# Kernel optimization log

Measured on AMD Instinct MI355X. Metric: run time of the kernel, lower is better.

The kernel has to match this reference:

```python
import jax, jax.numpy as jnp
import numpy as np

N_ANCH = 100800   # 3 * (160^2 + 80^2 + 40^2), YOLOv5 @ 1280
NUM_CLS = 80
IMG_HW = 1280
MAX_DETS = 300    # fixed padding for jit-compatible NMS output
OUT = 224
SCORE_THRESH = 0.1
IOU_THRESH = 0.45
ALLOWED = jnp.array([1, 2, 3, 4, 6, 8, 17, 18, 44], dtype=jnp.int32)
MEAN = jnp.array([0.485, 0.456, 0.406], dtype=jnp.float32).reshape(1, 3, 1, 1)
STD = jnp.array([0.229, 0.224, 0.225], dtype=jnp.float32).reshape(1, 3, 1, 1)


def setup_inputs() -> dict:
    key = jax.random.key(0)
    k1, k2, k3, k4, k5 = jax.random.split(key, 5)
    # realistic YOLO-style raw predictions: cx,cy in-image, modest w,h, gaussian class logits
    cxcy = jax.random.uniform(k1, (1, 2, N_ANCH), dtype=jnp.float32) * IMG_HW
    wh = jax.random.uniform(k2, (1, 2, N_ANCH), dtype=jnp.float32) * 256.0 + 8.0
    obj = jax.random.uniform(k3, (1, 1, N_ANCH), dtype=jnp.float32)
    logits = jax.random.normal(k4, (1, NUM_CLS, N_ANCH), dtype=jnp.float32)
    raw_pred = jnp.concatenate([cxcy, wh, obj, logits], axis=1)  # [1, 5+C, N]
    image = jax.random.uniform(k5, (1, 3, IMG_HW, IMG_HW), dtype=jnp.float32)
    return {"raw_pred": raw_pred, "image": image}


def _pairwise_iou(b):
    # b: [K,4] xyxy
    area = (b[:, 2] - b[:, 0]) * (b[:, 3] - b[:, 1])
    lt = jnp.maximum(b[:, None, :2], b[None, :, :2])
    rb = jnp.minimum(b[:, None, 2:], b[None, :, 2:])
    wh = jnp.clip(rb - lt, 0.0)
    inter = wh[..., 0] * wh[..., 1]
    union = area[:, None] + area[None, :] - inter
    return inter / jnp.maximum(union, 1e-9)


def _nms_keep(iou, valid):
    # greedy NMS over score-sorted boxes; returns boolean keep mask [K]
    K = iou.shape[0]
    idx = jnp.arange(K)

    def body(i, keep):
        suppress = keep[i] & (iou[i] > IOU_THRESH) & (idx > i)
        return keep & ~suppress

    return jax.lax.fori_loop(0, K, body, valid)


def _roi_align(image_chw, boxes):
    # torchvision roi_align, aligned=True, one sample per bin at the bin center
    # (sampling_ratio fixed to 1; see notes). image_chw: [3,H,W], boxes: [M,4]
    C, H, W = image_chw.shape
    grid = (jnp.arange(OUT, dtype=jnp.float32) + 0.5) / OUT  # fractional bin centers

    def one(box):
        x1, y1, x2, y2 = box
        xs = x1 - 0.5 + grid * (x2 - x1)  # [OUT], aligned=True half-pixel offset
        ys = y1 - 0.5 + grid * (y2 - y1)
        vx = (xs >= -1.0) & (xs <= W)
        vy = (ys >= -1.0) & (ys <= H)
        xc = jnp.clip(xs, 0.0, W - 1)
        yc = jnp.clip(ys, 0.0, H - 1)
        x0 = jnp.floor(xc).astype(jnp.int32)
        y0 = jnp.floor(yc).astype(jnp.int32)
        x1i = jnp.minimum(x0 + 1, W - 1)
        y1i = jnp.minimum(y0 + 1, H - 1)
        lx = xc - x0
        ly = yc - y0
        # bilinear gather: [3, OUT, OUT]
        v00 = image_chw[:, y0[:, None], x0[None, :]]
        v01 = image_chw[:, y0[:, None], x1i[None, :]]
        v10 = image_chw[:, y1i[:, None], x0[None, :]]
        v11 = image_chw[:, y1i[:, None], x1i[None, :]]
        top = v00 * (1.0 - lx) + v01 * lx
        bot = v10 * (1.0 - lx) + v11 * lx
        val = top * (1.0 - ly)[None, :, None] + bot * ly[None, :, None]
        return jnp.where(vy[None, :, None] & vx[None, None, :], val, 0.0)

    return jax.vmap(one)(boxes)


def _forward(raw_pred, image):
    x = raw_pred[0].T  # [N, 5+C]
    cx, cy, w, h = x[:, 0], x[:, 1], x[:, 2], x[:, 3]
    boxes = jnp.stack([cx - w / 2, cy - h / 2, cx + w / 2, cy + h / 2], axis=1)
    cls_logits = x[:, 5:]
    scores = cls_logits.max(axis=1)
    classes = cls_logits.argmax(axis=1).astype(jnp.int32) + 1
    # score + allowed-class filter (mask form)
    mask = (scores > SCORE_THRESH) & jnp.isin(classes, ALLOWED)
    masked_scores = jnp.where(mask, scores, jnp.finfo(scores.dtype).min)
    top_scores, top_idx = jax.lax.top_k(masked_scores, MAX_DETS)  # sorted desc
    top_boxes = boxes[top_idx]
    top_classes = classes[top_idx]
    valid = mask[top_idx]
    # greedy NMS over padded top-K candidates
    keep = _nms_keep(_pairwise_iou(top_boxes), valid)
    final_boxes = jnp.where(keep[:, None], top_boxes, 0.0)
    final_scores = jnp.where(keep, top_scores, 0.0)
    final_classes = jnp.where(keep, top_classes, 0)
    # crops: full image first, then RoIAlign crops, normalized once
    full_crop = jax.image.resize(image, (1, 3, OUT, OUT), method='linear', antialias=False)
    roi_crops = _roi_align(image[0], final_boxes)  # [K,3,224,224]
    roi_crops = jnp.where(keep[:, None, None, None], roi_crops, 0.0)
    all_crops = jnp.concatenate([full_crop, roi_crops], axis=0)  # [K+1,3,224,224]
    all_crops = (all_crops - MEAN) / STD
    return final_boxes, final_scores, final_classes, all_crops, keep


def reference(raw_pred, image):
    return _forward(raw_pred, image)
```

## Files before the change

kernel.cpp:

```cpp
#include <hip/hip_runtime.h>
#include <stdint.h>

#define N_ANCH   100800
#define NUM_CLS  80
#define IMG_HW   1280
#define MAX_DETS 300
#define OUTSZ    224
#define CAND_CAP 4096
#define LIST_CAP 16384

#define OFF_BOXES   0
#define OFF_SCORES  1200
#define OFF_CLASSES 1500
#define OFF_CROPS   1800
#define CROPS_ELEMS (301 * 3 * 224 * 224)
#define OFF_KEEP    (OFF_CROPS + CROPS_ELEMS)

#define SC_CNT    0
#define SC_CAND   64

typedef float f32x4 __attribute__((ext_vector_type(4)));

__device__ __forceinline__ uint32_t fkey(float f) {
    uint32_t u = __float_as_uint(f);
    return (u & 0x80000000u) ? ~u : (u | 0x80000000u);
}
__device__ __forceinline__ float unfkey(uint32_t k) {
    uint32_t u = (k & 0x80000000u) ? (k & 0x7fffffffu) : ~k;
    return __uint_as_float(u);
}

__global__ void k_score(const float* __restrict__ rp,
                        unsigned long long* __restrict__ cand,
                        uint32_t* __restrict__ cnt) {
    int gid = blockIdx.x * 256 + threadIdx.x;
    int grp = gid >> 3;
    int cp  = gid & 7;
    bool in = (grp < N_ANCH / 4);
    int a4 = in ? grp * 4 : 0;

    float best[4] = {-3.402823466e38f, -3.402823466e38f, -3.402823466e38f, -3.402823466e38f};
    int   bc[4]   = {0, 0, 0, 0};
    #pragma unroll
    for (int k = 0; k < 10; ++k) {
        int c = cp + 8 * k;
        float4 v = *(const float4*)&rp[(size_t)(5 + c) * N_ANCH + a4];
        if (v.x > best[0]) { best[0] = v.x; bc[0] = c; }
        if (v.y > best[1]) { best[1] = v.y; bc[1] = c; }
        if (v.z > best[2]) { best[2] = v.z; bc[2] = c; }
        if (v.w > best[3]) { best[3] = v.w; bc[3] = c; }
    }
    #pragma unroll
    for (int m = 1; m < 8; m <<= 1) {
        #pragma unroll
        for (int j = 0; j < 4; ++j) {
            float ob = __shfl_xor(best[j], m);
            int   oc = __shfl_xor(bc[j], m);
            if (ob > best[j] || (ob == best[j] && oc < bc[j])) { best[j] = ob; bc[j] = oc; }
        }
    }

    const unsigned long long AM =
        (1ULL << 1) | (1ULL << 2) | (1ULL << 3) | (1ULL << 4) | (1ULL << 6) |
        (1ULL << 8) | (1ULL << 17) | (1ULL << 18) | (1ULL << 44);
    unsigned long long pk[4];
    int cnt_loc = 0;
    bool lead = (cp == 0) && in;
    #pragma unroll
    for (int k = 0; k < 4; ++k) {
        int cls = bc[k] + 1;
        bool mk = lead && (best[k] > 0.1f) && (cls < 64) && ((AM >> cls) & 1ULL);
        uint32_t low = ((0x1FFFFu ^ (uint32_t)(a4 + k)) << 7) | (uint32_t)cls;
        pk[k] = mk ? (((unsigned long long)fkey(best[k]) << 32) | low) : 0ull;
        cnt_loc += mk ? 1 : 0;
    }

    int inc = cnt_loc;
    #pragma unroll
    for (int d = 1; d < 64; d <<= 1) {
        int vv = __shfl_up(inc, d);
        if ((threadIdx.x & 63) >= d) inc += vv;
    }
    int total = __shfl(inc, 63);
    uint32_t base = 0u;
    if (((threadIdx.x & 63) == 63) && total > 0) base = atomicAdd(cnt, (uint32_t)total);
    base = (uint32_t)__shfl((int)base, 63);
    uint32_t pos = base + (uint32_t)(inc - cnt_loc);
    #pragma unroll
    for (int k = 0; k < 4; ++k) {
        if (pk[k]) {
            if (pos < LIST_CAP) cand[pos] = pk[k];
            ++pos;
        }
    }
}

__global__ void __launch_bounds__(1024) k_detect(const float* __restrict__ rp,
                                                 const unsigned long long* __restrict__ cand,
                                                 const uint32_t* __restrict__ cnt_p,
                                                 float* __restrict__ out) {
    __shared__ uint32_t lhist[16384];
    __shared__ uint32_t ssum[1024];
    __shared__ uint32_t swave[16];
    __shared__ int      sh_thr;
    __shared__ uint32_t s_cnt;
    __shared__ unsigned long long sb[CAND_CAP];
    __shared__ unsigned long long top[MAX_DETS];
    __shared__ float sbx[MAX_DETS][4];
    __shared__ float sscore[MAX_DETS];
    __shared__ int   scls[MAX_DETS];
    __shared__ __align__(8) uint32_t sup[MAX_DETS][10];
    __shared__ __align__(8) uint32_t kw[10];
    __shared__ __align__(8) uint32_t rnz[10];
    int t = threadIdx.x;
    int nl = min((int)(*cnt_p), LIST_CAP);

    #pragma unroll
    for (int i = 0; i < 16; ++i) lhist[t + i * 1024] = 0u;
    if (t == 0) s_cnt = 0u;
    __syncthreads();
    for (int i = t; i < nl; i += 1024)
        atomicAdd(&lhist[(uint32_t)(cand[i] >> 50)], 1u);
    __syncthreads();

    const uint4* h4 = (const uint4*)(&lhist[t * 16]);
    uint4 v0 = h4[0], v1 = h4[1], v2 = h4[2], v3 = h4[3];
    uint32_t s = v0.x + v0.y + v0.z + v0.w + v1.x + v1.y + v1.z + v1.w +
                 v2.x + v2.y + v2.z + v2.w + v3.x + v3.y + v3.z + v3.w;
    ssum[t] = s;
    uint32_t ws = s;
    #pragma unroll
    for (int m = 32; m; m >>= 1) ws += __shfl_xor(ws, m);
    if ((t & 63) == 0) swave[t >> 6] = ws;
    __syncthreads();
    if (t == 0) {
        uint32_t acc = 0; int wsel = -1;
        for (int w = 15; w >= 0; --w) {
            uint32_t v = swave[w];
            if (acc + v >= (uint32_t)MAX_DETS) { wsel = w; break; }
            acc += v;
        }
        int thr = 0;
        if (wsel >= 0) {
            int tsel = -1;
            for (int tg = wsel * 64 + 63; tg >= wsel * 64; --tg) {
                uint32_t v = ssum[tg];
                if (acc + v >= (uint32_t)MAX_DETS) { tsel = tg; break; }
                acc += v;
            }
            for (int b = tsel * 16 + 15; b >= tsel * 16; --b) {
                acc += lhist[b];
                if (acc >= (uint32_t)MAX_DETS) { thr = b; break; }
            }
        }
        sh_thr = thr;
    }
    __syncthreads();

    uint32_t thr = (uint32_t)sh_thr;
    for (int i = t; i < nl; i += 1024) {
        unsigned long long key = cand[i];
        if ((uint32_t)(key >> 50) >= thr) {
            uint32_t pos = atomicAdd(&s_cnt, 1u);
            if (pos < CAND_CAP) sb[pos] = key;
        }
    }
    __syncthreads();
    int n = min((int)s_cnt, CAND_CAP);

    if (t < MAX_DETS) top[t] = 0ull;
    for (int i = t; i < MAX_DETS * 10; i += 1024) ((uint32_t*)sup)[i] = 0u;
    if (t < 10) { kw[t] = 0u; rnz[t] = 0u; }
    __syncthreads();

    for (int i = t; i < n; i += 1024) {
        unsigned long long key = sb[i];
        int rank = 0;
        for (int j = 0; j < n; ++j) rank += (sb[j] > key) ? 1 : 0;
        if (rank < MAX_DETS) top[rank] = key;
    }
    __syncthreads();

    if (t < MAX_DETS) {
        unsigned long long key = top[t];
        bool valid = (key != 0ull);
        float score = 0.f; int cls = 0;
        float b0 = 0.f, b1 = 0.f, b2 = 0.f, b3 = 0.f;
        if (valid) {
            uint32_t low = (uint32_t)key;
            uint32_t a = 0x1FFFFu ^ ((low >> 7) & 0x1FFFFu);
            cls = (int)(low & 0x7Fu);
            score = unfkey((uint32_t)(key >> 32));
            float cx = rp[a], cy = rp[N_ANCH + a];
            float w = rp[2 * N_ANCH + a], h = rp[3 * N_ANCH + a];
            b0 = cx - w * 0.5f; b1 = cy - h * 0.5f;
            b2 = cx + w * 0.5f; b3 = cy + h * 0.5f;
            atomicOr(&kw[t >> 5], 1u << (t & 31));
        }
        sbx[t][0] = b0; sbx[t][1] = b1; sbx[t][2] = b2; sbx[t][3] = b3;
        sscore[t] = score; scls[t] = cls;
    }
    __syncthreads();

    for (int p = t; p < MAX_DETS * MAX_DETS; p += 1024) {
        int i = p / MAX_DETS, j = p % MAX_DETS;
        if (j > i) {
            float ax1 = sbx[i][0], ay1 = sbx[i][1], ax2 = sbx[i][2], ay2 = sbx[i][3];
            float bx1 = sbx[j][0], by1 = sbx[j][1], bx2 = sbx[j][2], by2 = sbx[j][3];
            float areaA = (ax2 - ax1) * (ay2 - ay1);
            float areaB = (bx2 - bx1) * (by2 - by1);
            float ltx = fmaxf(ax1, bx1), lty = fmaxf(ay1, by1);
            float rbx = fminf(ax2, bx2), rby = fminf(ay2, by2);
            float iw = fmaxf(rbx - ltx, 0.f), ih = fmaxf(rby - lty, 0.f);
            float inter = iw * ih;
            float uni = areaA + areaB - inter;
            float iou = inter / fmaxf(uni, 1e-9f);
            if (iou > 0.45f) {
                atomicOr(&sup[i][j >> 5], 1u << (j & 31));
                atomicOr(&rnz[i >> 5], 1u << (i & 31));
            }
        }
    }
    __syncthreads();

    if (t == 0) {
        unsigned long long kwr[5], rnzr[5];
        const unsigned long long* kq = (const unsigned long long*)kw;
        const unsigned long long* rq = (const unsigned long long*)rnz;
        #pragma unroll
        for (int w = 0; w < 5; ++w) { kwr[w] = kq[w]; rnzr[w] = rq[w]; }
        #pragma unroll
        for (int sblk = 0; sblk < 5; ++sblk) {
            int lim = (sblk == 4) ? (MAX_DETS - 4 * 64) : 64;
            for (int i2 = 0; i2 < lim; ++i2) {
                if (((kwr[sblk] >> i2) & 1ull) && ((rnzr[sblk] >> i2) & 1ull)) {
                    int i = sblk * 64 + i2;
                    const unsigned long long* row = (const unsigned long long*)&sup[i][0];
                    kwr[0] &= ~row[0]; kwr[1] &= ~row[1]; kwr[2] &= ~row[2];
                    kwr[3] &= ~row[3]; kwr[4] &= ~row[4];
                }
            }
        }
        unsigned long long* kqo = (unsigned long long*)kw;
        #pragma unroll
        for (int w = 0; w < 5; ++w) kqo[w] = kwr[w];
    }
    __syncthreads();

    if (t < MAX_DETS) {
        bool kp = (kw[t >> 5] >> (t & 31)) & 1u;
        out[OFF_BOXES + t * 4 + 0] = kp ? sbx[t][0] : 0.f;
        out[OFF_BOXES + t * 4 + 1] = kp ? sbx[t][1] : 0.f;
        out[OFF_BOXES + t * 4 + 2] = kp ? sbx[t][2] : 0.f;
        out[OFF_BOXES + t * 4 + 3] = kp ? sbx[t][3] : 0.f;
        out[OFF_SCORES + t]  = kp ? sscore[t] : 0.f;
        out[OFF_CLASSES + t] = kp ? (float)scls[t] : 0.f;
        out[OFF_KEEP + t]    = kp ? 1.f : 0.f;
    }
}

#define RPB    16
#define TROWS  22
#define TPITCH 272

__device__ __forceinline__ float bilerp_g(const float* __restrict__ ch, float xc, float yc) {
    int x0 = (int)floorf(xc), y0 = (int)floorf(yc);
    int x1 = min(x0 + 1, IMG_HW - 1), y1 = min(y0 + 1, IMG_HW - 1);
    float lx = xc - (float)x0, ly = yc - (float)y0;
    float v00 = ch[y0 * IMG_HW + x0], v01 = ch[y0 * IMG_HW + x1];
    float v10 = ch[y1 * IMG_HW + x0], v11 = ch[y1 * IMG_HW + x1];
    return (v00 * (1.f - lx) + v01 * lx) * (1.f - ly) +
           (v10 * (1.f - lx) + v11 * lx) * ly;
}

__global__ void k_crops(const float* __restrict__ img, float* __restrict__ out) {
    __shared__ float tile[TROWS * TPITCH];
    int bx = blockIdx.x;
    int nc = blockIdx.y;
    int n = nc / 3, c = nc - n * 3;
    int t = threadIdx.x;
    int rl = t / 14;
    int xs14 = t - rl * 14;
    bool act = (t < 224);
    int oy = bx * RPB + rl;
    int ox0 = xs14 * 16;
    const float meanv[3] = {0.485f, 0.456f, 0.406f};
    const float stdv[3]  = {0.229f, 0.224f, 0.225f};
    float mean = meanv[c], rstd = 1.0f / stdv[c];
    const float* ch = img + (size_t)c * (IMG_HW * IMG_HW);
    f32x4 v[4];

    if (n == 0) {
        if (act) {
            float sy = ((float)oy + 0.5f) * (1280.0f / 224.0f) - 0.5f;
            #pragma unroll
            for (int k = 0; k < 16; ++k) {
                float sx = ((float)(ox0 + k) + 0.5f) * (1280.0f / 224.0f) - 0.5f;
                v[k >> 2][k & 3] = (bilerp_g(ch, sx, sy) - mean) * rstd;
            }
        }
    } else {
        float kp = out[OFF_KEEP + (n - 1)];
        if (kp == 0.f) {
            float z = (0.f - mean) * rstd;
            #pragma unroll
            for (int k4 = 0; k4 < 4; ++k4) v[k4] = (f32x4){z, z, z, z};
        } else {
            float4 bxv = *(const float4*)&out[OFF_BOXES + (n - 1) * 4];
            float x1b = bxv.x, y1b = bxv.y, x2b = bxv.z, y2b = bxv.w;
            float bw = x2b - x1b, bh = y2b - y1b;
            float ys0 = y1b - 0.5f + (((float)(bx * RPB) + 0.5f) / 224.0f) * bh;
            float ys1 = y1b - 0.5f + (((float)(bx * RPB + RPB - 1) + 0.5f) / 224.0f) * bh;
            int iy_min = (int)floorf(fminf(fmaxf(ys0, 0.f), 1279.f));
            int iy_max = min((int)floorf(fminf(fmaxf(ys1, 0.f), 1279.f)) + 1, IMG_HW - 1);
            float xs0 = x1b - 0.5f + (0.5f / 224.0f) * bw;
            float xs1 = x1b - 0.5f + (223.5f / 224.0f) * bw;
            int ix_min = (int)floorf(fminf(fmaxf(xs0, 0.f), 1279.f));
            int ix_max = min((int)floorf(fminf(fmaxf(xs1, 0.f), 1279.f)) + 1, IMG_HW - 1);
            int ix_al = ix_min & ~3;
            int rows = iy_max - iy_min + 1;
            int w4   = (ix_max - ix_al + 4) >> 2;
            int total = rows * w4;
            float winv = 1.0f / (float)w4;
            for (int i = t; i < total; i += 256) {
                int r  = (int)((float)i * winv);
                int cc = i - r * w4;
                if (cc < 0)        { r--; cc += w4; }
                else if (cc >= w4) { r++; cc -= w4; }
                int gy = iy_min + r;
                int px = ix_al + cc * 4;
                const float* src = ch + (size_t)gy * IMG_HW + px;
                float4 val;
                if ((px + 3 < IMG_HW) || (gy < IMG_HW - 1) || (c < 2)) {
                    val = *(const float4*)src;
                } else {
                    val.x = src[0];
                    val.y = src[min(1, IMG_HW - 1 - px)];
                    val.z = src[min(2, IMG_HW - 1 - px)];
                    val.w = src[min(3, IMG_HW - 1 - px)];
                }
                *(float4*)&tile[r * TPITCH + cc * 4] = val;
            }
            __syncthreads();
            if (act) {
                float gy = ((float)oy + 0.5f) / 224.0f;
                float ys = y1b - 0.5f + gy * bh;
                bool vy = (ys >= -1.0f) && (ys <= 1280.0f);
                float ycl = fminf(fmaxf(ys, 0.f), 1279.f);
                int y0 = (int)floorf(ycl);
                int y1i = min(y0 + 1, IMG_HW - 1);
                float ly = ycl - (float)y0;
                int ry0 = (y0 - iy_min) * TPITCH - ix_al;
                int ry1 = (y1i - iy_min) * TPITCH - ix_al;
                #pragma unroll
                for (int k = 0; k < 16; ++k) {
                    float gx = ((float)(ox0 + k) + 0.5f) / 224.0f;
                    float xs = x1b - 0.5f + gx * bw;
                    bool vx = (xs >= -1.0f) && (xs <= 1280.0f);
                    float xcl = fminf(fmaxf(xs, 0.f), 1279.f);
                    int x0 = (int)floorf(xcl);
                    int x1i = min(x0 + 1, IMG_HW - 1);
                    float lx = xcl - (float)x0;
                    float v00 = tile[ry0 + x0], v01 = tile[ry0 + x1i];
                    float v10 = tile[ry1 + x0], v11 = tile[ry1 + x1i];
                    float val = (v00 * (1.f - lx) + v01 * lx) * (1.f - ly) +
                                (v10 * (1.f - lx) + v11 * lx) * ly;
                    if (!(vx && vy)) val = 0.f;
                    v[k >> 2][k & 3] = (val - mean) * rstd;
                }
            }
        }
    }
    if (act) {
        float* dst = out + OFF_CROPS + (size_t)nc * (OUTSZ * OUTSZ) + (size_t)oy * OUTSZ + ox0;
        #pragma unroll
        for (int k4 = 0; k4 < 4; ++k4)
            __builtin_nontemporal_store(v[k4], (f32x4*)(dst + k4 * 4));
    }
}

extern "C" void kernel_launch(void* const* d_in, const int* in_sizes, int n_in,
                              void* d_out, int out_size, void* d_ws, size_t ws_size,
                              hipStream_t stream) {
    (void)in_sizes; (void)n_in; (void)out_size; (void)d_ws; (void)ws_size;
    const float* rp  = (const float*)d_in[0];
    const float* img = (const float*)d_in[1];
    float* out = (float*)d_out;
    char* sbase = (char*)d_out + (size_t)OFF_CROPS * sizeof(float);
    uint32_t* cnt = (uint32_t*)(sbase + SC_CNT);
    unsigned long long* cand = (unsigned long long*)(sbase + SC_CAND);

    hipMemsetAsync(sbase, 0, 64, stream);
    k_score<<<(N_ANCH / 4 * 8 + 255) / 256, 256, 0, stream>>>(rp, cand, cnt);
    k_detect<<<1, 1024, 0, stream>>>(rp, cand, cnt, out);
    dim3 grid(14, 903);
    k_crops<<<grid, 256, 0, stream>>>(img, out);
}
```

Before: 391.6 us.

## Remap crop kernel to four outputs per thread and add interior fast path

Crop blocks now cover 256 threads times four contiguous outputs, replacing sixteen outputs per thread over sixteen rows. The grid grows from 14 to 49 blocks per channel-crop, and the staged shared tile shrinks to about six source rows. This raises parallelism and cuts per-thread register use. A branch-free interior path using FMA-based bilinear interpolation skips clamping and validity checks when the box lies fully inside the image. The cost is more blocks and more redundant tile staging per output row.

Result: faster. 344.0 us (-12.2%).

```diff
diff --git a/kernel.cpp b/kernel.cpp
--- a/kernel.cpp
+++ b/kernel.cpp
@@ -259,8 +259,7 @@
     }
 }
 
-#define RPB    16
-#define TROWS  22
+#define TROWS  8
 #define TPITCH 272
 
 __device__ __forceinline__ float bilerp_g(const float* __restrict__ ch, float xc, float yc) {
@@ -279,42 +278,40 @@
     int nc = blockIdx.y;
     int n = nc / 3, c = nc - n * 3;
     int t = threadIdx.x;
-    int rl = t / 14;
-    int xs14 = t - rl * 14;
-    bool act = (t < 224);
-    int oy = bx * RPB + rl;
-    int ox0 = xs14 * 16;
+    int q = bx * 256 + t;
+    int oy = q / 56;
+    int ox0 = (q - oy * 56) * 4;
     const float meanv[3] = {0.485f, 0.456f, 0.406f};
     const float stdv[3]  = {0.229f, 0.224f, 0.225f};
     float mean = meanv[c], rstd = 1.0f / stdv[c];
     const float* ch = img + (size_t)c * (IMG_HW * IMG_HW);
-    f32x4 v[4];
+    f32x4 v;
 
     if (n == 0) {
-        if (act) {
-            float sy = ((float)oy + 0.5f) * (1280.0f / 224.0f) - 0.5f;
-            #pragma unroll
-            for (int k = 0; k < 16; ++k) {
-                float sx = ((float)(ox0 + k) + 0.5f) * (1280.0f / 224.0f) - 0.5f;
-                v[k >> 2][k & 3] = (bilerp_g(ch, sx, sy) - mean) * rstd;
-            }
+        float sy = ((float)oy + 0.5f) * (1280.0f / 224.0f) - 0.5f;
+        #pragma unroll
+        for (int k = 0; k < 4; ++k) {
+            float sx = ((float)(ox0 + k) + 0.5f) * (1280.0f / 224.0f) - 0.5f;
+            v[k] = (bilerp_g(ch, sx, sy) - mean) * rstd;
         }
     } else {
         float kp = out[OFF_KEEP + (n - 1)];
         if (kp == 0.f) {
             float z = (0.f - mean) * rstd;
-            #pragma unroll
-            for (int k4 = 0; k4 < 4; ++k4) v[k4] = (f32x4){z, z, z, z};
+            v = (f32x4){z, z, z, z};
         } else {
             float4 bxv = *(const float4*)&out[OFF_BOXES + (n - 1) * 4];
             float x1b = bxv.x, y1b = bxv.y, x2b = bxv.z, y2b = bxv.w;
             float bw = x2b - x1b, bh = y2b - y1b;
-            float ys0 = y1b - 0.5f + (((float)(bx * RPB) + 0.5f) / 224.0f) * bh;
-            float ys1 = y1b - 0.5f + (((float)(bx * RPB + RPB - 1) + 0.5f) / 224.0f) * bh;
+            float x1bm = x1b - 0.5f, y1bm = y1b - 0.5f;
+            int oy_s = (bx * 256) / 56;
+            int oy_e = (bx * 256 + 255) / 56;
+            float ys0 = y1bm + (((float)oy_s + 0.5f) / 224.0f) * bh;
+            float ys1 = y1bm + (((float)oy_e + 0.5f) / 224.0f) * bh;
+            float xs0 = x1bm + (0.5f / 224.0f) * bw;
+            float xs1 = x1bm + (223.5f / 224.0f) * bw;
             int iy_min = (int)floorf(fminf(fmaxf(ys0, 0.f), 1279.f));
             int iy_max = min((int)floorf(fminf(fmaxf(ys1, 0.f), 1279.f)) + 1, IMG_HW - 1);
-            float xs0 = x1b - 0.5f + (0.5f / 224.0f) * bw;
-            float xs1 = x1b - 0.5f + (223.5f / 224.0f) * bw;
             int ix_min = (int)floorf(fminf(fmaxf(xs0, 0.f), 1279.f));
             int ix_max = min((int)floorf(fminf(fmaxf(xs1, 0.f), 1279.f)) + 1, IMG_HW - 1);
             int ix_al = ix_min & ~3;
@@ -342,9 +339,33 @@
                 *(float4*)&tile[r * TPITCH + cc * 4] = val;
             }
             __syncthreads();
-            if (act) {
-                float gy = ((float)oy + 0.5f) / 224.0f;
-                float ys = y1b - 0.5f + gy * bh;
+
+            bool interior = (xs0 >= 0.0f) && (xs1 < 1279.0f) &&
+                            (ys0 >= 0.0f) && (ys1 < 1279.0f);
+            float gy = ((float)oy + 0.5f) / 224.0f;
+            float ys = y1bm + gy * bh;
+            if (interior) {
+                float y0f = floorf(ys);
+                float ly = ys - y0f;
+                int y0 = (int)y0f;
+                int ry0 = (y0 - iy_min) * TPITCH - ix_al;
+                int ry1 = ry0 + TPITCH;
+                #pragma unroll
+                for (int k = 0; k < 4; ++k) {
+                    float gx = ((float)(ox0 + k) + 0.5f) / 224.0f;
+                    float xs = x1bm + gx * bw;
+                    float x0f = floorf(xs);
+                    float lx = xs - x0f;
+                    int x0 = (int)x0f;
+                    int a0 = ry0 + x0, a1 = ry1 + x0;
+                    float t00 = tile[a0], t01 = tile[a0 + 1];
+                    float t10 = tile[a1], t11 = tile[a1 + 1];
+                    float top = __builtin_fmaf(lx, t01 - t00, t00);
+                    float bot = __builtin_fmaf(lx, t11 - t10, t10);
+                    float val = __builtin_fmaf(ly, bot - top, top);
+                    v[k] = (val - mean) * rstd;
+                }
+            } else {
                 bool vy = (ys >= -1.0f) && (ys <= 1280.0f);
                 float ycl = fminf(fmaxf(ys, 0.f), 1279.f);
                 int y0 = (int)floorf(ycl);
@@ -353,9 +374,9 @@
                 int ry0 = (y0 - iy_min) * TPITCH - ix_al;
                 int ry1 = (y1i - iy_min) * TPITCH - ix_al;
                 #pragma unroll
-                for (int k = 0; k < 16; ++k) {
+                for (int k = 0; k < 4; ++k) {
                     float gx = ((float)(ox0 + k) + 0.5f) / 224.0f;
-                    float xs = x1b - 0.5f + gx * bw;
+                    float xs = x1bm + gx * bw;
                     bool vx = (xs >= -1.0f) && (xs <= 1280.0f);
                     float xcl = fminf(fmaxf(xs, 0.f), 1279.f);
                     int x0 = (int)floorf(xcl);
@@ -366,17 +387,13 @@
                     float val = (v00 * (1.f - lx) + v01 * lx) * (1.f - ly) +
                                 (v10 * (1.f - lx) + v11 * lx) * ly;
                     if (!(vx && vy)) val = 0.f;
-                    v[k >> 2][k & 3] = (val - mean) * rstd;
+                    v[k] = (val - mean) * rstd;
                 }
             }
         }
     }
-    if (act) {
-        float* dst = out + OFF_CROPS + (size_t)nc * (OUTSZ * OUTSZ) + (size_t)oy * OUTSZ + ox0;
-        #pragma unroll
-        for (int k4 = 0; k4 < 4; ++k4)
-            __builtin_nontemporal_store(v[k4], (f32x4*)(dst + k4 * 4));
-    }
+    f32x4* dst = (f32x4*)(out + OFF_CROPS + (size_t)nc * (OUTSZ * OUTSZ) + oy * OUTSZ + ox0);
+    __builtin_nontemporal_store(v, dst);
 }
 
 extern "C" void kernel_launch(void* const* d_in, const int* in_sizes, int n_in,
@@ -393,6 +410,6 @@
     hipMemsetAsync(sbase, 0, 64, stream);
     k_score<<<(N_ANCH / 4 * 8 + 255) / 256, 256, 0, stream>>>(rp, cand, cnt);
     k_detect<<<1, 1024, 0, stream>>>(rp, cand, cnt, out);
-    dim3 grid(14, 903);
+    dim3 grid(49, 903);
     k_crops<<<grid, 256, 0, stream>>>(img, out);
 }
```
